# Kernel tuning notes

Hardware: AMD Instinct MI355X
Metric: run time of the kernel (lower is better)

The kernel has to match this reference:

```python
import jax, jax.numpy as jnp
import numpy as np

DIM = 1024
N_STATE = 64
T, B = 512, 32


def _xavier(key, shape):
    fan_out, fan_in = shape
    limit = np.sqrt(6.0 / (fan_in + fan_out)).astype(np.float32)
    return jax.random.uniform(key, shape, jnp.float32, -limit, limit)


def setup_inputs() -> dict:
    key = jax.random.key(0)
    ks = jax.random.split(key, 5)
    return {
        "x": jax.random.normal(ks[0], (T, B, DIM), jnp.float32),
        "S": jnp.zeros((B, N_STATE, N_STATE), jnp.float32),
        "W_k": _xavier(ks[1], (N_STATE, DIM)),
        "W_v": _xavier(ks[2], (N_STATE, DIM)),
        "W_q": _xavier(ks[3], (N_STATE, DIM)),
        "W_alpha": _xavier(ks[4], (N_STATE, DIM)),
        "d_alpha": jnp.full((N_STATE,), 0.1, jnp.float32),
        "b_alpha": jnp.full((N_STATE,), 2.0, jnp.float32),
    }


def reference(x, S, W_k, W_v, W_q, W_alpha, d_alpha, b_alpha):
    # Precompute all projections as batched GEMMs: [T,B,n_state]
    k = jnp.einsum("tbd,nd->tbn", x, W_k)
    v = jnp.einsum("tbd,nd->tbn", x, W_v)
    q = jnp.einsum("tbd,nd->tbn", x, W_q)
    ax = jnp.einsum("tbd,nd->tbn", x, W_alpha)

    def step(S, inp):
        k_t, v_t, q_t, ax_t = inp  # each [B, n_state]
        retrieved = jnp.einsum("bij,bj->bi", S, k_t)          # S @ k
        alpha = jax.nn.sigmoid(ax_t + d_alpha * retrieved + b_alpha)
        # S = alpha * S + (1 - alpha) * outer(v, k); alpha gates rows
        S_new = alpha[:, :, None] * S + (1.0 - alpha)[:, :, None] * (
            v_t[:, :, None] * k_t[:, None, :]
        )
        h = jnp.einsum("bij,bj->bi", S_new, q_t)              # S @ q
        out_t = h * jax.nn.silu(h)                             # self-gated output
        return S_new, out_t

    S_final, output = jax.lax.scan(step, S, (k, v, q, ax))
    return output, S_final
```

## Files before the change

kernel.cpp:

```cpp
#include <hip/hip_runtime.h>
#include <hip/hip_bf16.h>

#define T_STEPS 512
#define BATCH 32
#define NST 64
#define DIM 1024

typedef _Float16 f16x8 __attribute__((ext_vector_type(8)));
typedef _Float16 f16x4 __attribute__((ext_vector_type(4)));
typedef _Float16 f16x2 __attribute__((ext_vector_type(2)));
typedef float f32x4 __attribute__((ext_vector_type(4)));

__device__ __forceinline__ void gl_lds16(const void* g, void* l) {
  __builtin_amdgcn_global_load_lds(
      (const __attribute__((address_space(1))) void*)g,
      (__attribute__((address_space(3))) void*)l, 16, 0, 0);
}

__global__ __launch_bounds__(256) void wconv(
    const float* __restrict__ Wk, const float* __restrict__ Wv,
    const float* __restrict__ Wq, const float* __restrict__ Wa,
    _Float16* __restrict__ Wc) {
  const int n = blockIdx.x;
  const int g = n >> 6, r = n & 63;
  const float* W = (g == 0) ? Wk : (g == 1) ? Wq : (g == 2) ? Wv : Wa;
  float4 v = *(const float4*)(W + (size_t)r * DIM + threadIdx.x * 4);
  f16x4 h = {(_Float16)v.x, (_Float16)v.y, (_Float16)v.z, (_Float16)v.w};
  *(f16x4*)(Wc + (size_t)n * DIM + threadIdx.x * 4) = h;
}

__global__ __launch_bounds__(256) void proj_gemm(
    const float* __restrict__ x, const _Float16* __restrict__ Wc,
    _Float16* __restrict__ projh) {
  const int m0 = blockIdx.x * 64;
  const int n0 = blockIdx.y * 128;
  const int tid = threadIdx.x;
  const int lane = tid & 63, wv = tid >> 6;
  const int wm = wv >> 1, wn = wv & 1;
  const int fm = lane & 15, fq = lane >> 4;

  __shared__ __align__(16) _Float16 Al[64 * 40];
  __shared__ __align__(16) _Float16 Bl[2][128 * 32];

  const int bro = wv * 32 + (lane >> 2);
  const int bchunk = (lane & 3) ^ ((lane >> 3) & 3);
  const _Float16* gB = Wc + (size_t)(n0 + bro) * DIM + bchunk * 8;
  const int bl_off = bro * 32 + (lane & 3) * 8;

  const int arow = tid >> 2;
  const int acol = (tid & 3) * 8;
  const float* gA = x + (size_t)(m0 + arow) * DIM + acol;

  f32x4 acc[2][4];
#pragma unroll
  for (int mi = 0; mi < 2; ++mi)
#pragma unroll
    for (int ni = 0; ni < 4; ++ni) acc[mi][ni] = (f32x4){0.f, 0.f, 0.f, 0.f};

#define STAGE_B(buf, k0)                                       \
  {                                                            \
    _Pragma("unroll") for (int j = 0; j < 2; ++j)              \
        gl_lds16(gB + (size_t)j * 16 * DIM + (k0),             \
                 &Bl[buf][bl_off + j * 16 * 32]);              \
  }
  float4 xa, xb;
#define LOAD_A(k0)                          \
  {                                         \
    xa = *(const float4*)(gA + (k0));       \
    xb = *(const float4*)(gA + (k0) + 4);   \
  }

  STAGE_B(0, 0);
  LOAD_A(0);
  const int aswz = (fq ^ ((fm >> 1) & 3)) * 8;
  for (int kt = 0; kt < 32; ++kt) {
    __syncthreads();
    f16x8 ah;
    ah[0] = (_Float16)xa.x; ah[1] = (_Float16)xa.y;
    ah[2] = (_Float16)xa.z; ah[3] = (_Float16)xa.w;
    ah[4] = (_Float16)xb.x; ah[5] = (_Float16)xb.y;
    ah[6] = (_Float16)xb.z; ah[7] = (_Float16)xb.w;
    *(f16x8*)&Al[arow * 40 + acol] = ah;
    __syncthreads();
    if (kt + 1 < 32) {
      LOAD_A(kt * 32 + 32);
      STAGE_B((kt + 1) & 1, kt * 32 + 32);
    }
    f16x8 afr[2], bfr[4];
#pragma unroll
    for (int mi = 0; mi < 2; ++mi)
      afr[mi] = *(const f16x8*)&Al[(wm * 32 + mi * 16 + fm) * 40 + fq * 8];
#pragma unroll
    for (int ni = 0; ni < 4; ++ni) {
      const int row = wn * 64 + ni * 16 + fm;
      bfr[ni] = *(const f16x8*)&Bl[kt & 1][row * 32 + aswz];
    }
#pragma unroll
    for (int mi = 0; mi < 2; ++mi)
#pragma unroll
      for (int ni = 0; ni < 4; ++ni)
        acc[mi][ni] =
            __builtin_amdgcn_mfma_f32_16x16x32_f16(afr[mi], bfr[ni], acc[mi][ni], 0, 0, 0);
  }
#undef STAGE_B
#undef LOAD_A

#pragma unroll
  for (int mi = 0; mi < 2; ++mi)
#pragma unroll
    for (int ni = 0; ni < 4; ++ni) {
      const int gcol = n0 + wn * 64 + ni * 16 + fm;
      const int pcol = gcol < 128 ? gcol
                     : (gcol < 192 ? 128 + 2 * (gcol - 128) : 129 + 2 * (gcol - 192));
#pragma unroll
      for (int r = 0; r < 4; ++r) {
        const int grow = m0 + wm * 32 + mi * 16 + fq * 4 + r;
        projh[(size_t)grow * 256 + pcol] = (_Float16)acc[mi][ni][r];
      }
    }
}

__device__ __forceinline__ float red16(float x) {
  int v = __builtin_amdgcn_update_dpp(0, __float_as_int(x), 0xB1, 0xF, 0xF, true);
  x += __int_as_float(v);
  v = __builtin_amdgcn_update_dpp(0, __float_as_int(x), 0x4E, 0xF, 0xF, true);
  x += __int_as_float(v);
  v = __builtin_amdgcn_update_dpp(0, __float_as_int(x), 0x124, 0xF, 0xF, true);
  x += __int_as_float(v);
  v = __builtin_amdgcn_update_dpp(0, __float_as_int(x), 0x128, 0xF, 0xF, true);
  x += __int_as_float(v);
  return x;
}

__global__ __launch_bounds__(256) void scan_kernel(
    const _Float16* __restrict__ projh, const float* __restrict__ S0,
    const float* __restrict__ d_alpha, const float* __restrict__ b_alpha,
    float* __restrict__ out, float* __restrict__ Sout) {
  const int b = blockIdx.x >> 2;
  const int rg = blockIdx.x & 3;
  const int tid = threadIdx.x;
  const int c = tid & 15;
  const int r = rg * 16 + (tid >> 4);
  const int j0 = c * 4;

  __shared__ __align__(16) _Float16 lbuf[2 * 2048];

  float s[4];
  {
    float4 v = *(const float4*)(S0 + ((size_t)b * NST + r) * NST + j0);
    s[0] = v.x; s[1] = v.y; s[2] = v.z; s[3] = v.w;
  }
  const float da = d_alpha[r];
  const float ba = b_alpha[r];

  const _Float16* gp = projh + (size_t)b * 256;
  const int lidx = (tid >> 5) * 256 + (tid & 31) * 8;
#define GADDR(ch) (gp + (size_t)((ch) * 8 + (tid >> 5)) * (BATCH * 256) + (tid & 31) * 8)

  float4 rA;
  rA = *(const float4*)GADDR(0); *(float4*)(lbuf + lidx) = rA;
  rA = *(const float4*)GADDR(1); *(float4*)(lbuf + 2048 + lidx) = rA;
  rA = *(const float4*)GADDR(2);
  __syncthreads();

  f16x4 kf[2], qf[2];
  f16x2 vaf[2];
#define PREF(tn)                                                           \
  {                                                                        \
    const int pp = (tn)&1;                                                 \
    const _Float16* Pn = lbuf + (((tn) >> 3) & 1) * 2048 + ((tn)&7) * 256; \
    kf[pp] = *(const f16x4*)(Pn + j0);                                     \
    qf[pp] = *(const f16x4*)(Pn + 64 + j0);                                \
    vaf[pp] = *(const f16x2*)(Pn + 128 + 2 * r);                           \
  }

  PREF(0);
  for (int ch = 0; ch < 64; ++ch) {
#pragma unroll
    for (int si = 0; si < 8; ++si) {
      const int t = ch * 8 + si;
      const int p = t & 1;
      if (t + 1 < T_STEPS) PREF(t + 1);

      const float k0 = (float)kf[p][0], k1 = (float)kf[p][1];
      const float k2 = (float)kf[p][2], k3 = (float)kf[p][3];
      const float q0 = (float)qf[p][0], q1 = (float)qf[p][1];
      const float q2 = (float)qf[p][2], q3 = (float)qf[p][3];
      const float vi = (float)vaf[p][0];
      const float axv = (float)vaf[p][1];

      const float pa = fmaf(s[0], k0, s[1] * k1);
      const float pb = fmaf(s[2], k2, s[3] * k3);
      const float rr = red16(pa + pb);

      float z = fmaf(da, rr, axv + ba);
      z = fminf(fmaxf(z, -30.f), 30.f);
      const float e = __expf(-z);
      const float al = __builtin_amdgcn_rcpf(1.f + e);
      const float cc = (e * vi) * al;

      s[0] = fmaf(al, s[0], cc * k0);
      s[1] = fmaf(al, s[1], cc * k1);
      s[2] = fmaf(al, s[2], cc * k2);
      s[3] = fmaf(al, s[3], cc * k3);
      const float ha = fmaf(s[0], q0, s[1] * q1);
      const float hb = fmaf(s[2], q2, s[3] * q3);
      const float h = red16(ha + hb);

      if (c == 0) {
        const float sg = __builtin_amdgcn_rcpf(1.f + __expf(-h));
        out[((size_t)t * BATCH + b) * NST + r] = h * h * sg;
      }
    }
    if (ch + 2 < 64) {
      __syncthreads();
      *(float4*)(lbuf + (ch & 1) * 2048 + lidx) = rA;
      if (ch + 3 < 64) rA = *(const float4*)GADDR(ch + 3);
      __syncthreads();
    }
  }
#undef PREF
#undef GADDR

  float4 o = {s[0], s[1], s[2], s[3]};
  *(float4*)(Sout + ((size_t)b * NST + r) * NST + j0) = o;
}

extern "C" void kernel_launch(void* const* d_in, const int* in_sizes, int n_in,
                              void* d_out, int out_size, void* d_ws, size_t ws_size,
                              hipStream_t stream) {
  const float* x  = (const float*)d_in[0];
  const float* S0 = (const float*)d_in[1];
  const float* Wk = (const float*)d_in[2];
  const float* Wv = (const float*)d_in[3];
  const float* Wq = (const float*)d_in[4];
  const float* Wa = (const float*)d_in[5];
  const float* da = (const float*)d_in[6];
  const float* ba = (const float*)d_in[7];

  float* out  = (float*)d_out;
  float* Sout = out + (size_t)T_STEPS * BATCH * NST;
  _Float16* projh = (_Float16*)d_ws;
  _Float16* Wc = (_Float16*)((char*)d_ws + (size_t)16384 * 256 * 2);

  wconv<<<256, 256, 0, stream>>>(Wk, Wv, Wq, Wa, Wc);
  dim3 ggrid(16384 / 64, 2);
  proj_gemm<<<ggrid, 256, 0, stream>>>(x, Wc, projh);
  scan_kernel<<<4 * BATCH, 256, 0, stream>>>(projh, S0, da, ba, out, Sout);
}
```

Baseline: 226.3 us.

## Register-resident GEMM without LDS and algebraic single-reduction-chain scan step

The projection GEMM drops its LDS staging. Each 2-wave block now computes 64 rows by all 256 columns, with A and B fragments loaded straight from global memory into register ring buffers (4-deep for A, 2-deep for B). The scan kernel drops its LDS double-buffer and syncthreads, prefetching 8 timesteps of k/q/v/a directly from global into registers. It also rewrites h as al*(S·q) + cc*(k·q), so the three dot-product reductions become independent and can overlap instead of running serially. The sigmoid now uses exp2 with the scale folded in beforehand. In exchange, GEMM occupancy is much lower (256 blocks of 128 threads, very high register use), and the scan loads become many small uncoalesced global reads.

After: 338.4 us. 49.5% more time.

```diff
diff --git a/kernel.cpp b/kernel.cpp
--- a/kernel.cpp
+++ b/kernel.cpp
@@ -5,17 +5,12 @@
 #define BATCH 32
 #define NST 64
 #define DIM 1024
+#define LOG2E 1.44269504f
 
 typedef _Float16 f16x8 __attribute__((ext_vector_type(8)));
 typedef _Float16 f16x4 __attribute__((ext_vector_type(4)));
 typedef _Float16 f16x2 __attribute__((ext_vector_type(2)));
 typedef float f32x4 __attribute__((ext_vector_type(4)));
-
-__device__ __forceinline__ void gl_lds16(const void* g, void* l) {
-  __builtin_amdgcn_global_load_lds(
-      (const __attribute__((address_space(1))) void*)g,
-      (__attribute__((address_space(3))) void*)l, 16, 0, 0);
-}
 
 __global__ __launch_bounds__(256) void wconv(
     const float* __restrict__ Wk, const float* __restrict__ Wv,
@@ -29,93 +24,82 @@
   *(f16x4*)(Wc + (size_t)n * DIM + threadIdx.x * 4) = h;
 }
 
-__global__ __launch_bounds__(256) void proj_gemm(
+__global__ __launch_bounds__(128, 1) void proj_gemm(
     const float* __restrict__ x, const _Float16* __restrict__ Wc,
-    _Float16* __restrict__ projh) {
-  const int m0 = blockIdx.x * 64;
-  const int n0 = blockIdx.y * 128;
+    _Float16* __restrict__ P) {
   const int tid = threadIdx.x;
   const int lane = tid & 63, wv = tid >> 6;
-  const int wm = wv >> 1, wn = wv & 1;
   const int fm = lane & 15, fq = lane >> 4;
-
-  __shared__ __align__(16) _Float16 Al[64 * 40];
-  __shared__ __align__(16) _Float16 Bl[2][128 * 32];
-
-  const int bro = wv * 32 + (lane >> 2);
-  const int bchunk = (lane & 3) ^ ((lane >> 3) & 3);
-  const _Float16* gB = Wc + (size_t)(n0 + bro) * DIM + bchunk * 8;
-  const int bl_off = bro * 32 + (lane & 3) * 8;
-
-  const int arow = tid >> 2;
-  const int acol = (tid & 3) * 8;
-  const float* gA = x + (size_t)(m0 + arow) * DIM + acol;
-
-  f32x4 acc[2][4];
+  const int m0 = blockIdx.x * 64 + wv * 32;
+
+  const float* gA0 = x + (size_t)(m0 + fm) * DIM + fq * 8;
+  const float* gA1 = gA0 + (size_t)16 * DIM;
+  const _Float16* gBb = Wc + (size_t)fm * DIM + fq * 8;
+
+  f32x4 acc[2][16];
 #pragma unroll
   for (int mi = 0; mi < 2; ++mi)
 #pragma unroll
-    for (int ni = 0; ni < 4; ++ni) acc[mi][ni] = (f32x4){0.f, 0.f, 0.f, 0.f};
-
-#define STAGE_B(buf, k0)                                       \
+    for (int ni = 0; ni < 16; ++ni) acc[mi][ni] = (f32x4){0.f, 0.f, 0.f, 0.f};
+
+  float4 xa[4][2][2];
+  f16x8 bf[2][16];
+
+#define LDA(slot, kt)                                          \
   {                                                            \
-    _Pragma("unroll") for (int j = 0; j < 2; ++j)              \
-        gl_lds16(gB + (size_t)j * 16 * DIM + (k0),             \
-                 &Bl[buf][bl_off + j * 16 * 32]);              \
-  }
-  float4 xa, xb;
-#define LOAD_A(k0)                          \
-  {                                         \
-    xa = *(const float4*)(gA + (k0));       \
-    xb = *(const float4*)(gA + (k0) + 4);   \
-  }
-
-  STAGE_B(0, 0);
-  LOAD_A(0);
-  const int aswz = (fq ^ ((fm >> 1) & 3)) * 8;
+    xa[slot][0][0] = *(const float4*)(gA0 + (kt) * 32);        \
+    xa[slot][0][1] = *(const float4*)(gA0 + (kt) * 32 + 4);    \
+    xa[slot][1][0] = *(const float4*)(gA1 + (kt) * 32);        \
+    xa[slot][1][1] = *(const float4*)(gA1 + (kt) * 32 + 4);    \
+  }
+#define LDB(buf, kt)                                                          \
+  {                                                                           \
+    _Pragma("unroll") for (int ni = 0; ni < 16; ++ni)                         \
+        bf[buf][ni] = *(const f16x8*)(gBb + (size_t)(ni * 16) * DIM + (kt) * 32); \
+  }
+
+  LDA(0, 0); LDA(1, 1); LDA(2, 2); LDA(3, 3);
+  LDB(0, 0); LDB(1, 1);
+
+#pragma unroll
   for (int kt = 0; kt < 32; ++kt) {
-    __syncthreads();
-    f16x8 ah;
-    ah[0] = (_Float16)xa.x; ah[1] = (_Float16)xa.y;
-    ah[2] = (_Float16)xa.z; ah[3] = (_Float16)xa.w;
-    ah[4] = (_Float16)xb.x; ah[5] = (_Float16)xb.y;
-    ah[6] = (_Float16)xb.z; ah[7] = (_Float16)xb.w;
-    *(f16x8*)&Al[arow * 40 + acol] = ah;
-    __syncthreads();
-    if (kt + 1 < 32) {
-      LOAD_A(kt * 32 + 32);
-      STAGE_B((kt + 1) & 1, kt * 32 + 32);
-    }
-    f16x8 afr[2], bfr[4];
-#pragma unroll
-    for (int mi = 0; mi < 2; ++mi)
-      afr[mi] = *(const f16x8*)&Al[(wm * 32 + mi * 16 + fm) * 40 + fq * 8];
-#pragma unroll
-    for (int ni = 0; ni < 4; ++ni) {
-      const int row = wn * 64 + ni * 16 + fm;
-      bfr[ni] = *(const f16x8*)&Bl[kt & 1][row * 32 + aswz];
-    }
-#pragma unroll
-    for (int mi = 0; mi < 2; ++mi)
-#pragma unroll
-      for (int ni = 0; ni < 4; ++ni)
-        acc[mi][ni] =
-            __builtin_amdgcn_mfma_f32_16x16x32_f16(afr[mi], bfr[ni], acc[mi][ni], 0, 0, 0);
-  }
-#undef STAGE_B
-#undef LOAD_A
+    const int slot = kt & 3, buf = kt & 1;
+    f16x8 af[2];
+#pragma unroll
+    for (int mi = 0; mi < 2; ++mi) {
+      af[mi][0] = (_Float16)xa[slot][mi][0].x;
+      af[mi][1] = (_Float16)xa[slot][mi][0].y;
+      af[mi][2] = (_Float16)xa[slot][mi][0].z;
+      af[mi][3] = (_Float16)xa[slot][mi][0].w;
+      af[mi][4] = (_Float16)xa[slot][mi][1].x;
+      af[mi][5] = (_Float16)xa[slot][mi][1].y;
+      af[mi][6] = (_Float16)xa[slot][mi][1].z;
+      af[mi][7] = (_Float16)xa[slot][mi][1].w;
+    }
+#pragma unroll
+    for (int ni = 0; ni < 16; ++ni) {
+      acc[0][ni] = __builtin_amdgcn_mfma_f32_16x16x32_f16(af[0], bf[buf][ni],
+                                                          acc[0][ni], 0, 0, 0);
+      acc[1][ni] = __builtin_amdgcn_mfma_f32_16x16x32_f16(af[1], bf[buf][ni],
+                                                          acc[1][ni], 0, 0, 0);
+    }
+    if (kt + 4 < 32) LDA(slot, kt + 4);
+    if (kt + 2 < 32) LDB(buf, kt + 2);
+  }
+#undef LDA
+#undef LDB
 
 #pragma unroll
   for (int mi = 0; mi < 2; ++mi)
 #pragma unroll
-    for (int ni = 0; ni < 4; ++ni) {
-      const int gcol = n0 + wn * 64 + ni * 16 + fm;
+    for (int ni = 0; ni < 16; ++ni) {
+      const int gcol = ni * 16 + fm;
       const int pcol = gcol < 128 ? gcol
                      : (gcol < 192 ? 128 + 2 * (gcol - 128) : 129 + 2 * (gcol - 192));
 #pragma unroll
       for (int r = 0; r < 4; ++r) {
-        const int grow = m0 + wm * 32 + mi * 16 + fq * 4 + r;
-        projh[(size_t)grow * 256 + pcol] = (_Float16)acc[mi][ni][r];
+        const int grow = m0 + mi * 16 + fq * 4 + r;
+        P[(size_t)grow * 256 + pcol] = (_Float16)acc[mi][ni][r];
       }
     }
 }
@@ -133,7 +117,7 @@
 }
 
 __global__ __launch_bounds__(256) void scan_kernel(
-    const _Float16* __restrict__ projh, const float* __restrict__ S0,
+    const _Float16* __restrict__ P, const float* __restrict__ S0,
     const float* __restrict__ d_alpha, const float* __restrict__ b_alpha,
     float* __restrict__ out, float* __restrict__ Sout) {
   const int b = blockIdx.x >> 2;
@@ -143,8 +127,6 @@
   const int r = rg * 16 + (tid >> 4);
   const int j0 = c * 4;
 
-  __shared__ __align__(16) _Float16 lbuf[2 * 2048];
-
   float s[4];
   {
     float4 v = *(const float4*)(S0 + ((size_t)b * NST + r) * NST + j0);
@@ -152,75 +134,62 @@
   }
   const float da = d_alpha[r];
   const float ba = b_alpha[r];
-
-  const _Float16* gp = projh + (size_t)b * 256;
-  const int lidx = (tid >> 5) * 256 + (tid & 31) * 8;
-#define GADDR(ch) (gp + (size_t)((ch) * 8 + (tid >> 5)) * (BATCH * 256) + (tid & 31) * 8)
-
-  float4 rA;
-  rA = *(const float4*)GADDR(0); *(float4*)(lbuf + lidx) = rA;
-  rA = *(const float4*)GADDR(1); *(float4*)(lbuf + 2048 + lidx) = rA;
-  rA = *(const float4*)GADDR(2);
-  __syncthreads();
-
-  f16x4 kf[2], qf[2];
-  f16x2 vaf[2];
-#define PREF(tn)                                                           \
-  {                                                                        \
-    const int pp = (tn)&1;                                                 \
-    const _Float16* Pn = lbuf + (((tn) >> 3) & 1) * 2048 + ((tn)&7) * 256; \
-    kf[pp] = *(const f16x4*)(Pn + j0);                                     \
-    qf[pp] = *(const f16x4*)(Pn + 64 + j0);                                \
-    vaf[pp] = *(const f16x2*)(Pn + 128 + 2 * r);                           \
-  }
-
-  PREF(0);
-  for (int ch = 0; ch < 64; ++ch) {
-#pragma unroll
-    for (int si = 0; si < 8; ++si) {
-      const int t = ch * 8 + si;
-      const int p = t & 1;
-      if (t + 1 < T_STEPS) PREF(t + 1);
-
-      const float k0 = (float)kf[p][0], k1 = (float)kf[p][1];
-      const float k2 = (float)kf[p][2], k3 = (float)kf[p][3];
-      const float q0 = (float)qf[p][0], q1 = (float)qf[p][1];
-      const float q2 = (float)qf[p][2], q3 = (float)qf[p][3];
-      const float vi = (float)vaf[p][0];
-      const float axv = (float)vaf[p][1];
-
-      const float pa = fmaf(s[0], k0, s[1] * k1);
-      const float pb = fmaf(s[2], k2, s[3] * k3);
-      const float rr = red16(pa + pb);
-
-      float z = fmaf(da, rr, axv + ba);
-      z = fminf(fmaxf(z, -30.f), 30.f);
-      const float e = __expf(-z);
-      const float al = __builtin_amdgcn_rcpf(1.f + e);
-      const float cc = (e * vi) * al;
-
-      s[0] = fmaf(al, s[0], cc * k0);
-      s[1] = fmaf(al, s[1], cc * k1);
-      s[2] = fmaf(al, s[2], cc * k2);
-      s[3] = fmaf(al, s[3], cc * k3);
-      const float ha = fmaf(s[0], q0, s[1] * q1);
-      const float hb = fmaf(s[2], q2, s[3] * q3);
-      const float h = red16(ha + hb);
-
-      if (c == 0) {
-        const float sg = __builtin_amdgcn_rcpf(1.f + __expf(-h));
-        out[((size_t)t * BATCH + b) * NST + r] = h * h * sg;
-      }
-    }
-    if (ch + 2 < 64) {
-      __syncthreads();
-      *(float4*)(lbuf + (ch & 1) * 2048 + lidx) = rA;
-      if (ch + 3 < 64) rA = *(const float4*)GADDR(ch + 3);
-      __syncthreads();
-    }
-  }
-#undef PREF
-#undef GADDR
+  const float mda = -da * LOG2E;
+
+  const _Float16* gp = P + (size_t)b * 256;
+
+  f16x4 kf[8], qf[8];
+  f16x2 vaf[8];
+#define LD_T(t)                                              \
+  {                                                          \
+    const _Float16* Pt = gp + (size_t)(t) * (BATCH * 256);   \
+    kf[(t) & 7] = *(const f16x4*)(Pt + j0);                  \
+    qf[(t) & 7] = *(const f16x4*)(Pt + 64 + j0);             \
+    vaf[(t) & 7] = *(const f16x2*)(Pt + 128 + 2 * r);        \
+  }
+
+  LD_T(0); LD_T(1); LD_T(2); LD_T(3);
+  LD_T(4); LD_T(5); LD_T(6); LD_T(7);
+
+#pragma unroll 8
+  for (int t = 0; t < T_STEPS; ++t) {
+    const int p = t & 7;
+    const float k0 = (float)kf[p][0], k1 = (float)kf[p][1];
+    const float k2 = (float)kf[p][2], k3 = (float)kf[p][3];
+    const float q0 = (float)qf[p][0], q1 = (float)qf[p][1];
+    const float q2 = (float)qf[p][2], q3 = (float)qf[p][3];
+    const float vi = (float)vaf[p][0];
+    const float zcv = ((float)vaf[p][1] + ba) * (-LOG2E);
+    if (t + 8 < T_STEPS) LD_T(t + 8);
+
+    float pa = fmaf(s[0], k0, s[1] * k1);
+    float pb = fmaf(s[2], k2, s[3] * k3);
+    float ua = fmaf(s[0], q0, s[1] * q1);
+    float ub = fmaf(s[2], q2, s[3] * q3);
+    float ka = fmaf(k0, q0, k1 * q1);
+    float kb = fmaf(k2, q2, k3 * q3);
+    const float rr = red16(pa + pb);
+    const float uu = red16(ua + ub);
+    const float kq = red16(ka + kb);
+
+    float tt = fmaf(rr, mda, zcv);
+    tt = fminf(fmaxf(tt, -45.f), 45.f);
+    const float e = exp2f(tt);
+    const float al = __builtin_amdgcn_rcpf(1.f + e);
+    const float cc = (e * vi) * al;
+
+    s[0] = fmaf(al, s[0], cc * k0);
+    s[1] = fmaf(al, s[1], cc * k1);
+    s[2] = fmaf(al, s[2], cc * k2);
+    s[3] = fmaf(al, s[3], cc * k3);
+
+    const float h = fmaf(al, uu, cc * kq);
+    if (c == 0) {
+      const float sg = __builtin_amdgcn_rcpf(1.f + __expf(-h));
+      out[((size_t)t * BATCH + b) * NST + r] = h * h * sg;
+    }
+  }
+#undef LD_T
 
   float4 o = {s[0], s[1], s[2], s[3]};
   *(float4*)(Sout + ((size_t)b * NST + r) * NST + j0) = o;
@@ -240,11 +209,10 @@
 
   float* out  = (float*)d_out;
   float* Sout = out + (size_t)T_STEPS * BATCH * NST;
-  _Float16* projh = (_Float16*)d_ws;
-  _Float16* Wc = (_Float16*)((char*)d_ws + (size_t)16384 * 256 * 2);
+  _Float16* P = (_Float16*)d_ws;
+  _Float16* Wc = (_Float16*)((char*)d_ws + (size_t)8 * 1024 * 1024);
 
   wconv<<<256, 256, 0, stream>>>(Wk, Wv, Wq, Wa, Wc);
-  dim3 ggrid(16384 / 64, 2);
-  proj_gemm<<<ggrid, 256, 0, stream>>>(x, Wc, projh);
-  scan_kernel<<<4 * BATCH, 256, 0, stream>>>(projh, S0, da, ba, out, Sout);
-}
+  proj_gemm<<<256, 128, 0, stream>>>(x, Wc, P);
+  scan_kernel<<<4 * BATCH, 256, 0, stream>>>(P, S0, da, ba, out, Sout);
+}
```
